# Kernel tuning notes

Measured on AMD Instinct MI355X. Metric: run time of the kernel, lower is better.

Reference implementation:

```python
import jax, jax.numpy as jnp
import numpy as np
from functools import partial

B, N, T = 4, 10000, 128
E = 160000
H, C = 4, 64            # heads, out_channels per head
GAT_DIM = H * C         # 256
NEG_SLOPE = 0.2


def conv1d(x, w, b):
    # x: (M, Cin, L), w: (Cout, Cin, K), 'same' padding (pad=1 for k=3)
    y = jax.lax.conv_general_dilated(x, w, window_strides=(1,), padding=[(1, 1)],
                                     dimension_numbers=('NCH', 'OIH', 'NCH'))
    return y + b[None, :, None]


def maxpool2(x):
    # kernel=2, stride=2 over last axis
    return jax.lax.reduce_window(x, -jnp.inf, jax.lax.max,
                                 (1, 1, 2), (1, 1, 2), 'VALID')


def gat_layer_single(x, src, dst, W, att_s, att_d, bias):
    # x: (N, Fin); PyG GATConv with concat=True, self-loops already appended to src/dst
    n = x.shape[0]
    xl = (x @ W).reshape(n, H, C)                       # (N, H, C)
    a_s = jnp.sum(xl * att_s[None], axis=-1)            # (N, H)
    a_d = jnp.sum(xl * att_d[None], axis=-1)            # (N, H)
    e = jax.nn.leaky_relu(a_s[src] + a_d[dst], NEG_SLOPE)  # (E', H)
    emax = jax.ops.segment_max(e, dst, num_segments=n)     # (N, H)
    ex = jnp.exp(e - emax[dst])
    denom = jax.ops.segment_sum(ex, dst, num_segments=n)   # (N, H)
    alpha = ex / (denom[dst] + 1e-16)                       # (E', H)
    msg = xl[src] * alpha[..., None]                        # (E', H, C)
    out = jax.ops.segment_sum(msg, dst, num_segments=n)     # (N, H, C)
    return out.reshape(n, H * C) + bias


def setup_inputs() -> dict:
    key = jax.random.key(0)
    ks = jax.random.split(key, 24)
    rn = lambda k, sh, fan: jax.random.normal(k, sh, jnp.float32) / np.sqrt(fan)
    inp = {
        'x': jax.random.normal(ks[0], (B, N, T), jnp.float32),
        'edge_index': jax.random.randint(ks[1], (2, E), 0, N, jnp.int64),
        # temporal conv
        'cw1': rn(ks[2], (32, 1, 3), 3), 'cb1': jnp.zeros((32,), jnp.float32),
        'cw2': rn(ks[3], (64, 32, 3), 96), 'cb2': jnp.zeros((64,), jnp.float32),
        # GAT layer 0 (in=64)
        'W0': rn(ks[4], (64, GAT_DIM), 64), 'as0': rn(ks[5], (H, C), C), 'ad0': rn(ks[6], (H, C), C),
        'b0': jnp.zeros((GAT_DIM,), jnp.float32),
        # GAT layer 1 (in=256)
        'W1': rn(ks[7], (GAT_DIM, GAT_DIM), GAT_DIM), 'as1': rn(ks[8], (H, C), C), 'ad1': rn(ks[9], (H, C), C),
        'b1': jnp.zeros((GAT_DIM,), jnp.float32),
        # classification head 256->128->2
        'Wc1': rn(ks[10], (GAT_DIM, 128), GAT_DIM), 'bc1': jnp.zeros((128,), jnp.float32),
        'Wc2': rn(ks[11], (128, 2), 128), 'bc2': jnp.zeros((2,), jnp.float32),
        # attribution head 256->64->1
        'Wa1': rn(ks[12], (GAT_DIM, 64), GAT_DIM), 'ba1': jnp.zeros((64,), jnp.float32),
        'Wa2': rn(ks[13], (64, 1), 64), 'ba2': jnp.zeros((1,), jnp.float32),
    }
    return inp


def reference(x, edge_index, cw1, cb1, cw2, cb2, W0, as0, ad0, b0, W1, as1, ad1, b1,
              Wc1, bc1, Wc2, bc2, Wa1, ba1, Wa2, ba2):
    b, n, t = x.shape
    # ---- temporal conv over all B*N node signals ----
    xf = x.reshape(b * n, 1, t)
    h = jax.nn.relu(conv1d(xf, cw1, cb1))            # (BN, 32, T)
    h = maxpool2(h)                                  # (BN, 32, T//2)
    h = jax.nn.relu(conv1d(h, cw2, cb2))             # (BN, 64, T//2)
    feat = jnp.mean(h, axis=-1).reshape(b, n, 64)    # adaptive_avg_pool1d(1)
    # ---- GAT stack (self-loops appended, PyG default) ----
    src0, dst0 = edge_index[0], edge_index[1]
    loops = jnp.arange(n, dtype=src0.dtype)
    src = jnp.concatenate([src0, loops])
    dst = jnp.concatenate([dst0, loops])
    gat0 = jax.vmap(partial(gat_layer_single, src=src, dst=dst, W=W0, att_s=as0, att_d=ad0, bias=b0))
    gat1 = jax.vmap(partial(gat_layer_single, src=src, dst=dst, W=W1, att_s=as1, att_d=ad1, bias=b1))
    g = jax.nn.relu(gat0(feat))                      # (B, N, 256); dropout = identity (eval)
    g = jax.nn.relu(gat1(g))                         # (B, N, 256)
    # ---- heads ----
    pooled = jnp.mean(g, axis=1)                     # (B, 256)
    logits = jax.nn.relu(pooled @ Wc1 + bc1) @ Wc2 + bc2          # (B, 2)
    attr = jax.nn.sigmoid(jax.nn.relu(g @ Wa1 + ba1) @ Wa2 + ba2)  # (B, N, 1)
    return logits, attr[..., 0]
```

## Files before the change

### kernel.cpp

```cpp
#include <hip/hip_runtime.h>
#include <hip/hip_bf16.h>
#include <math.h>

typedef __hip_bfloat16 bf16;
typedef unsigned short u16;
typedef unsigned int u32;
typedef __attribute__((ext_vector_type(8))) short short8;
typedef __attribute__((ext_vector_type(4))) float f32x4;
typedef __attribute__((ext_vector_type(2))) float f32x2;

#define BATCH 4
#define NNODE 10000
#define TLEN 128
#define NEDGE 160000
#define GDIM 256
#define NHEAD 4

#define S_CW1 0
#define S_CB1 96
#define S_CB2 128
#define S_AS0 192
#define S_AD0 448
#define S_B0  704
#define S_AS1 960
#define S_AD1 1216
#define S_B1  1472
#define S_BC1 1728
#define S_WC2 1856
#define S_BC2 2112
#define S_BA1 2114
#define S_WA2 2178
#define S_BA2 2242
#define S_TOTAL 2243

__device__ __forceinline__ float prelu(float v) { return fmaxf(v, 0.f); }
__device__ __forceinline__ u16 f2b(float f) {
    union { float f; u32 u; } v; v.f = f;
    u32 r = v.u + 0x7FFF + ((v.u >> 16) & 1);
    return (u16)(r >> 16);
}
__device__ __forceinline__ float u2f(u16 u) {
    union { u32 u; float f; } v; v.u = ((u32)u) << 16;
    return v.f;
}
__device__ __forceinline__ float ldw(const void* p, int off, bool isbf) {
    return isbf ? u2f(((const u16*)p)[off]) : ((const float*)p)[off];
}

__device__ __forceinline__ bool probe_x_bf16(const void* xsrc) {
    int lane = threadIdx.x & 63;
    u16 h = ((const u16*)xsrc)[2 * lane];
    int e = (h >> 7) & 0xFF;
    unsigned long long m = __ballot(e >= 117 && e <= 130);
    return __popcll(m) >= 32;
}
__device__ __forceinline__ bool probe_ei64(const int* ei) {
    int lane = threadIdx.x & 63;
    int v = ei[2 * lane + 1];
    unsigned long long m = __ballot(v == 0);
    return __popcll(m) >= 56;
}

struct WPtrs { const void* p[20]; };

#define PRE_TBLK 665
__global__ __launch_bounds__(256) void k_pre(WPtrs wp, const void* __restrict__ xsrc,
        const int* __restrict__ ei, float* __restrict__ wbuf,
        u16* __restrict__ cw2r, u16* __restrict__ W0t, u16* __restrict__ W1t,
        u16* __restrict__ Wa1t, int* __restrict__ counts) {
    bool isbf = probe_x_bf16(xsrc);
    int b = blockIdx.x;
    if (b >= PRE_TBLK) {
        const int C2[16] = {0,96,128,192,448,704,960,1216,1472,1728,1856,2112,
                            2114,2178,2242,2243};
        const int SRC[15] = {0,1,3,5,6,7,9,10,11,13,14,15,17,18,19};
        int i = (b - PRE_TBLK) * 256 + threadIdx.x;
        if (i >= S_TOTAL) return;
        int j = 14;
        for (int t = 0; t < 15; ++t) { if (i < C2[t + 1]) { j = t; break; } }
        wbuf[i] = ldw(wp.p[SRC[j]], i - C2[j], isbf);
        return;
    }
    int i = b * 256 + threadIdx.x;
    if (i < 6144) {
        int c2 = i / 96, k = i - c2 * 96, s = k >> 5, ci = k & 31;
        cw2r[i] = f2b(ldw(wp.p[2], c2 * 96 + ci * 3 + s, isbf));
    }
    if (i < 16384) {
        int k = i >> 8, c = i & 255;
        W0t[c * 64 + k] = f2b(ldw(wp.p[4], k * 256 + c, isbf));
        int ka = i >> 6, ca = i & 63;
        Wa1t[ca * 256 + ka] = f2b(ldw(wp.p[16], ka * 64 + ca, isbf));
    }
    if (i < 65536) {
        int k = i >> 8, c = i & 255;
        W1t[c * 256 + k] = f2b(ldw(wp.p[8], k * 256 + c, isbf));
    }
    if (i < NEDGE + NNODE) {
        bool ei64 = probe_ei64(ei);
        int dst;
        if (i < NEDGE) dst = ei64 ? ei[2 * (NEDGE + i)] : ei[NEDGE + i];
        else dst = i - NEDGE;
        if (dst >= 0 && dst < NNODE) atomicAdd(&counts[dst], 1);
    }
}

__global__ __launch_bounds__(256) void k_scan1(const int* __restrict__ counts,
        int* __restrict__ cur, int* __restrict__ bsum) {
    __shared__ int buf[256];
    int tid = threadIdx.x;
    int i = blockIdx.x * 256 + tid;
    int v = (i < NNODE) ? counts[i] : 0;
    buf[tid] = v;
    __syncthreads();
    for (int off = 1; off < 256; off <<= 1) {
        int t = (tid >= off) ? buf[tid - off] : 0;
        __syncthreads();
        buf[tid] += t;
        __syncthreads();
    }
    if (i < NNODE) cur[i] = buf[tid];
    if (tid == 255) bsum[blockIdx.x] = buf[255];
}
__global__ __launch_bounds__(256) void k_scan3(const int* __restrict__ counts,
        int* __restrict__ cur, const int* __restrict__ bsum, int* __restrict__ row_ptr) {
    __shared__ int pre_s;
    int tid = threadIdx.x;
    if (tid == 0) {
        int s = 0;
        for (int j = 0; j < blockIdx.x; ++j) s += bsum[j];
        pre_s = s;
    }
    __syncthreads();
    int i = blockIdx.x * 256 + tid;
    if (i >= NNODE) return;
    int incl = cur[i] + pre_s;
    row_ptr[i + 1] = incl;
    cur[i] = incl - counts[i];
    if (i == 0) row_ptr[0] = 0;
}

#define HSTR 40
#define NPW 4
#define FILL_BLK 665
__global__ __launch_bounds__(256) void k_conv(const void* __restrict__ xsrc,
        const float* __restrict__ wbuf, const u16* __restrict__ cw2r,
        u16* __restrict__ featb, const int* __restrict__ ei,
        int* __restrict__ cur, int* __restrict__ col_src) {
    __shared__ __align__(16) float xs[4][132];
    __shared__ float w1s[96], b1s[32], b2s[64];
    __shared__ __align__(16) u16 hb[4][66 * HSTR];

    bool isbf = probe_x_bf16(xsrc);
    int tid = threadIdx.x;
    int wave = tid >> 6, lane = tid & 63;
    int node0 = blockIdx.x * (4 * NPW);

    int m = lane & 15, q = lane >> 4;
    short8 bfr[4][3];
    #pragma unroll
    for (int nt = 0; nt < 4; ++nt)
        #pragma unroll
        for (int sh = 0; sh < 3; ++sh)
            bfr[nt][sh] = *(const short8*)&cw2r[(nt * 16 + m) * 96 + sh * 32 + q * 8];

    if (tid < 96) w1s[tid] = wbuf[S_CW1 + tid];
    if (tid < 32) b1s[tid] = wbuf[S_CB1 + tid];
    if (tid < 64) b2s[tid] = wbuf[S_CB2 + tid];
    if (tid < 8) xs[tid >> 1][(tid & 1) ? 129 : 0] = 0.f;
    if (tid < 64) {
        int w = tid >> 4, idx = tid & 15;
        *(u32*)&hb[w][2 * idx] = 0;
        *(u32*)&hb[w][65 * HSTR + 2 * idx] = 0;
    }
    __syncthreads();

    float* xsw = xs[wave];
    u16* hw = &hb[wave][0];

    int d = m, uu = q;
    float wa0 = w1s[6 * d + 0], wa1 = w1s[6 * d + 1], wa2 = w1s[6 * d + 2];
    float wb0 = w1s[6 * d + 3], wb1 = w1s[6 * d + 4], wb2 = w1s[6 * d + 5];
    float ba = b1s[2 * d], bb = b1s[2 * d + 1];
    float b2vv[4];
    #pragma unroll
    for (int nt = 0; nt < 4; ++nt) b2vv[nt] = b2s[nt * 16 + m];

    int node = node0 + wave;
    u32 plo = 0; float2 pf = {0.f, 0.f};
    if (isbf) plo = ((const u32*)xsrc)[(size_t)node * 64 + lane];
    else      pf  = ((const float2*)xsrc)[(size_t)node * 64 + lane];

    for (int j = 0; j < NPW; ++j) {
        if (isbf) {
            xsw[1 + 2 * lane] = u2f((u16)(plo & 0xFFFF));
            xsw[2 + 2 * lane] = u2f((u16)(plo >> 16));
        } else {
            xsw[1 + 2 * lane] = pf.x;
            xsw[2 + 2 * lane] = pf.y;
        }
        if (j + 1 < NPW) {
            int nxt = node + 4;
            if (isbf) plo = ((const u32*)xsrc)[(size_t)nxt * 64 + lane];
            else      pf  = ((const float2*)xsrc)[(size_t)nxt * 64 + lane];
        }

        #pragma unroll
        for (int it = 0; it < 16; ++it) {
            int u = uu + 4 * it;
            int t0 = 2 * u;
            float2 xa = *(const float2*)&xsw[t0];
            float2 xb = *(const float2*)&xsw[t0 + 2];
            float x0 = xa.x, x1 = xa.y, x2 = xb.x, x3 = xb.y;
            f32x2 A = {x0, x1}, Bv = {x1, x2}, Cv = {x2, x3};
            f32x2 va = {ba, ba}; va += wa0 * A; va += wa1 * Bv; va += wa2 * Cv;
            f32x2 vb = {bb, bb}; vb += wb0 * A; vb += wb1 * Bv; vb += wb2 * Cv;
            float ha = fmaxf(fmaxf(va.x, va.y), 0.f);
            float hb2 = fmaxf(fmaxf(vb.x, vb.y), 0.f);
            __hip_bfloat162 hp2 = __float22bfloat162_rn(make_float2(ha, hb2));
            u32 pack; __builtin_memcpy(&pack, &hp2, 4);
            *(u32*)&hw[(u + 1) * HSTR + 2 * d] = pack;
        }

        float pc0 = 0.f, pc1 = 0.f, pc2 = 0.f, pc3 = 0.f;
        #pragma unroll
        for (int mt = 0; mt < 4; ++mt) {
            const u16* hr = &hw[(mt * 16 + m) * HSTR + q * 8];
            short8 a0 = *(const short8*)&hr[0 * HSTR];
            short8 a1 = *(const short8*)&hr[1 * HSTR];
            short8 a2 = *(const short8*)&hr[2 * HSTR];
            f32x4 c0 = {0.f,0.f,0.f,0.f}, c1 = {0.f,0.f,0.f,0.f};
            f32x4 c2 = {0.f,0.f,0.f,0.f}, c3 = {0.f,0.f,0.f,0.f};
            c0 = __builtin_amdgcn_mfma_f32_16x16x32_bf16(a0, bfr[0][0], c0, 0, 0, 0);
            c1 = __builtin_amdgcn_mfma_f32_16x16x32_bf16(a0, bfr[1][0], c1, 0, 0, 0);
            c2 = __builtin_amdgcn_mfma_f32_16x16x32_bf16(a0, bfr[2][0], c2, 0, 0, 0);
            c3 = __builtin_amdgcn_mfma_f32_16x16x32_bf16(a0, bfr[3][0], c3, 0, 0, 0);
            c0 = __builtin_amdgcn_mfma_f32_16x16x32_bf16(a1, bfr[0][1], c0, 0, 0, 0);
            c1 = __builtin_amdgcn_mfma_f32_16x16x32_bf16(a1, bfr[1][1], c1, 0, 0, 0);
            c2 = __builtin_amdgcn_mfma_f32_16x16x32_bf16(a1, bfr[2][1], c2, 0, 0, 0);
            c3 = __builtin_amdgcn_mfma_f32_16x16x32_bf16(a1, bfr[3][1], c3, 0, 0, 0);
            c0 = __builtin_amdgcn_mfma_f32_16x16x32_bf16(a2, bfr[0][2], c0, 0, 0, 0);
            c1 = __builtin_amdgcn_mfma_f32_16x16x32_bf16(a2, bfr[1][2], c1, 0, 0, 0);
            c2 = __builtin_amdgcn_mfma_f32_16x16x32_bf16(a2, bfr[2][2], c2, 0, 0, 0);
            c3 = __builtin_amdgcn_mfma_f32_16x16x32_bf16(a2, bfr[3][2], c3, 0, 0, 0);
            pc0 += prelu(c0[0] + b2vv[0]) + prelu(c0[1] + b2vv[0])
                 + prelu(c0[2] + b2vv[0]) + prelu(c0[3] + b2vv[0]);
            pc1 += prelu(c1[0] + b2vv[1]) + prelu(c1[1] + b2vv[1])
                 + prelu(c1[2] + b2vv[1]) + prelu(c1[3] + b2vv[1]);
            pc2 += prelu(c2[0] + b2vv[2]) + prelu(c2[1] + b2vv[2])
                 + prelu(c2[2] + b2vv[2]) + prelu(c2[3] + b2vv[2]);
            pc3 += prelu(c3[0] + b2vv[3]) + prelu(c3[1] + b2vv[3])
                 + prelu(c3[2] + b2vv[3]) + prelu(c3[3] + b2vv[3]);
        }
        pc0 += __shfl_xor(pc0, 16, 64); pc0 += __shfl_xor(pc0, 32, 64);
        pc1 += __shfl_xor(pc1, 16, 64); pc1 += __shfl_xor(pc1, 32, 64);
        pc2 += __shfl_xor(pc2, 16, 64); pc2 += __shfl_xor(pc2, 32, 64);
        pc3 += __shfl_xor(pc3, 16, 64); pc3 += __shfl_xor(pc3, 32, 64);
        float v = (q == 0) ? pc0 : (q == 1) ? pc1 : (q == 2) ? pc2 : pc3;
        int bb2 = node / NNODE, nn = node - bb2 * NNODE;
        featb[((size_t)nn * 4 + bb2) * 64 + lane] = f2b(v * (1.f / 64.f));

        node += 4;
    }

    if (blockIdx.x < FILL_BLK) {
        bool ei64 = probe_ei64(ei);
        int e = blockIdx.x * 256 + tid;
        if (e < NEDGE + NNODE) {
            int src, dst;
            if (e < NEDGE) {
                if (ei64) { src = ei[2 * e]; dst = ei[2 * (NEDGE + e)]; }
                else      { src = ei[e];     dst = ei[NEDGE + e]; }
            } else {
                src = dst = e - NEDGE;
            }
            if (dst >= 0 && dst < NNODE) {
                int pos = atomicAdd(&cur[dst], 1);
                if (pos >= 0 && pos < NEDGE + NNODE) col_src[pos] = src;
            }
        }
    }
}

template<int K>
__global__ __launch_bounds__(256) void k_gemm(const u16* __restrict__ A,
        const u16* __restrict__ Wt, const float* __restrict__ att_s_w,
        const float* __restrict__ att_d_w, u16* __restrict__ outb,
        float* __restrict__ a_s, float* __restrict__ a_d) {
    int wave = threadIdx.x >> 6, lane = threadIdx.x & 63;
    int row0 = (blockIdx.x * 4 + wave) * 16;
    int m = lane & 15, q = lane >> 4;
    f32x4 acc[16];
    #pragma unroll
    for (int nt = 0; nt < 16; ++nt) acc[nt] = {0.f, 0.f, 0.f, 0.f};
    for (int kc = 0; kc < K; kc += 32) {
        short8 a = *(const short8*)&A[(size_t)(row0 + m) * K + kc + q * 8];
        #pragma unroll
        for (int nt = 0; nt < 16; ++nt) {
            short8 b = *(const short8*)&Wt[(size_t)(nt * 16 + m) * K + kc + q * 8];
            acc[nt] = __builtin_amdgcn_mfma_f32_16x16x32_bf16(a, b, acc[nt], 0, 0, 0);
        }
    }
    #pragma unroll
    for (int nt = 0; nt < 16; ++nt) {
        #pragma unroll
        for (int r = 0; r < 4; ++r)
            outb[(size_t)(row0 + q * 4 + r) * 256 + nt * 16 + m] = f2b(acc[nt][r]);
    }
    float sh_s[4][4] = {{0}}, sh_d[4][4] = {{0}};
    #pragma unroll
    for (int nt = 0; nt < 16; ++nt) {
        int h = nt >> 2;
        int cc = (nt & 3) * 16 + m;
        float asw = att_s_w[h * 64 + cc];
        float adw = att_d_w[h * 64 + cc];
        #pragma unroll
        for (int r = 0; r < 4; ++r) {
            sh_s[h][r] += acc[nt][r] * asw;
            sh_d[h][r] += acc[nt][r] * adw;
        }
    }
    #pragma unroll
    for (int off = 1; off < 16; off <<= 1) {
        #pragma unroll
        for (int h = 0; h < 4; ++h)
            #pragma unroll
            for (int r = 0; r < 4; ++r) {
                sh_s[h][r] += __shfl_xor(sh_s[h][r], off, 64);
                sh_d[h][r] += __shfl_xor(sh_d[h][r], off, 64);
            }
    }
    if (m == 0) {
        #pragma unroll
        for (int r = 0; r < 4; ++r) {
            int row = row0 + q * 4 + r;
            float4 vs = {sh_s[0][r], sh_s[1][r], sh_s[2][r], sh_s[3][r]};
            float4 vd = {sh_d[0][r], sh_d[1][r], sh_d[2][r], sh_d[3][r]};
            *(float4*)&a_s[(size_t)row * 4] = vs;
            *(float4*)&a_d[(size_t)row * 4] = vd;
        }
    }
}

__global__ __launch_bounds__(256) void k_agg(const u16* __restrict__ xlb,
        const float* __restrict__ a_s, const float* __restrict__ a_d,
        const int* __restrict__ row_ptr, const int* __restrict__ col_src,
        const float* __restrict__ bias, u16* __restrict__ gb_out) {
    int wave = threadIdx.x >> 6, lane = threadIdx.x & 63;
    int dst = __builtin_amdgcn_readfirstlane(blockIdx.x * 2 + (wave >> 1));
    int bp = (wave & 1) * 2;
    int beg = __builtin_amdgcn_readfirstlane(row_ptr[dst]);
    int end = __builtin_amdgcn_readfirstlane(row_ptr[dst + 1]);

    int bl = lane >> 5;
    int s = lane & 31;
    int h = s >> 3;
    int b = bp + bl;
    int asoff = b * 4 + h;
    float advh = a_d[(size_t)dst * 16 + asoff];

    float m = -INFINITY, l = 0.f;
    float acc[8];
    #pragma unroll
    for (int k = 0; k < 8; ++k) acc[k] = 0.f;

    int i = beg;
    for (; i + 4 <= end; i += 4) {
        int s0 = min(max(col_src[i], 0), NNODE - 1);
        int s1 = min(max(col_src[i + 1], 0), NNODE - 1);
        int s2 = min(max(col_src[i + 2], 0), NNODE - 1);
        int s3 = min(max(col_src[i + 3], 0), NNODE - 1);
        float a0 = a_s[(size_t)s0 * 16 + asoff];
        float a1 = a_s[(size_t)s1 * 16 + asoff];
        float a2 = a_s[(size_t)s2 * 16 + asoff];
        float a3 = a_s[(size_t)s3 * 16 + asoff];
        short8 x0 = *(const short8*)&xlb[((size_t)s0 * 4 + b) * 256 + s * 8];
        short8 x1 = *(const short8*)&xlb[((size_t)s1 * 4 + b) * 256 + s * 8];
        short8 x2 = *(const short8*)&xlb[((size_t)s2 * 4 + b) * 256 + s * 8];
        short8 x3 = *(const short8*)&xlb[((size_t)s3 * 4 + b) * 256 + s * 8];
        float e0 = a0 + advh; e0 = (e0 >= 0.f) ? e0 : 0.2f * e0;
        float e1 = a1 + advh; e1 = (e1 >= 0.f) ? e1 : 0.2f * e1;
        float e2 = a2 + advh; e2 = (e2 >= 0.f) ? e2 : 0.2f * e2;
        float e3 = a3 + advh; e3 = (e3 >= 0.f) ? e3 : 0.2f * e3;
        float cmax = fmaxf(fmaxf(e0, e1), fmaxf(e2, e3));
        if (__any(cmax > m)) {
            float mn = fmaxf(m, cmax);
            float r = __expf(m - mn);
            m = mn;
            l *= r;
            #pragma unroll
            for (int k = 0; k < 8; ++k) acc[k] *= r;
        }
        float p0 = __expf(e0 - m); l += p0;
        #pragma unroll
        for (int k = 0; k < 8; ++k) acc[k] += p0 * u2f((u16)x0[k]);
        float p1 = __expf(e1 - m); l += p1;
        #pragma unroll
        for (int k = 0; k < 8; ++k) acc[k] += p1 * u2f((u16)x1[k]);
        float p2 = __expf(e2 - m); l += p2;
        #pragma unroll
        for (int k = 0; k < 8; ++k) acc[k] += p2 * u2f((u16)x2[k]);
        float p3 = __expf(e3 - m); l += p3;
        #pragma unroll
        for (int k = 0; k < 8; ++k) acc[k] += p3 * u2f((u16)x3[k]);
    }
    for (; i < end; ++i) {
        int s0 = min(max(col_src[i], 0), NNODE - 1);
        float a0 = a_s[(size_t)s0 * 16 + asoff];
        short8 x0 = *(const short8*)&xlb[((size_t)s0 * 4 + b) * 256 + s * 8];
        float e0 = a0 + advh; e0 = (e0 >= 0.f) ? e0 : 0.2f * e0;
        if (__any(e0 > m)) {
            float mn = fmaxf(m, e0);
            float r = __expf(m - mn);
            m = mn;
            l *= r;
            #pragma unroll
            for (int k = 0; k < 8; ++k) acc[k] *= r;
        }
        float p0 = __expf(e0 - m); l += p0;
        #pragma unroll
        for (int k = 0; k < 8; ++k) acc[k] += p0 * u2f((u16)x0[k]);
    }

    float rl = 1.f / (l + 1e-16f);
    short8 o;
    #pragma unroll
    for (int k = 0; k < 8; ++k)
        o[k] = (short)f2b(prelu(acc[k] * rl + bias[s * 8 + k]));
    *(short8*)&gb_out[((size_t)dst * 4 + b) * 256 + s * 8] = o;
}

__global__ __launch_bounds__(256) void k_attrpool(const u16* __restrict__ gb,
        const u16* __restrict__ Wa1t, const float* __restrict__ wbuf,
        float* __restrict__ out, float* __restrict__ pooled) {
    if (blockIdx.x >= 625) {
        int pb = blockIdx.x - 625;
        int b = pb >> 6;
        int chunk = pb & 63;
        int cch = threadIdx.x;
        int n0 = chunk * 157;
        int n1 = min(NNODE, n0 + 157);
        float acc = 0.f;
        int n = n0;
        for (; n + 4 <= n1; n += 4) {
            float v0 = u2f(gb[((size_t)n * 4 + b) * 256 + cch]);
            float v1 = u2f(gb[((size_t)(n + 1) * 4 + b) * 256 + cch]);
            float v2 = u2f(gb[((size_t)(n + 2) * 4 + b) * 256 + cch]);
            float v3 = u2f(gb[((size_t)(n + 3) * 4 + b) * 256 + cch]);
            acc += v0; acc += v1; acc += v2; acc += v3;
        }
        for (; n < n1; ++n)
            acc += u2f(gb[((size_t)n * 4 + b) * 256 + cch]);
        atomicAdd(&pooled[b * 256 + cch], acc);
        return;
    }
    int wave = threadIdx.x >> 6, lane = threadIdx.x & 63;
    int row0 = (blockIdx.x * 4 + wave) * 16;
    int m = lane & 15, q = lane >> 4;
    f32x4 acc[4];
    #pragma unroll
    for (int nt = 0; nt < 4; ++nt) acc[nt] = {0.f, 0.f, 0.f, 0.f};
    for (int kc = 0; kc < 256; kc += 32) {
        short8 a = *(const short8*)&gb[(size_t)(row0 + m) * 256 + kc + q * 8];
        #pragma unroll
        for (int nt = 0; nt < 4; ++nt) {
            short8 b = *(const short8*)&Wa1t[(size_t)(nt * 16 + m) * 256 + kc + q * 8];
            acc[nt] = __builtin_amdgcn_mfma_f32_16x16x32_bf16(a, b, acc[nt], 0, 0, 0);
        }
    }
    float part[4] = {0, 0, 0, 0};
    #pragma unroll
    for (int nt = 0; nt < 4; ++nt) {
        int col = nt * 16 + m;
        float ba1v = wbuf[S_BA1 + col];
        float wa2v = wbuf[S_WA2 + col];
        #pragma unroll
        for (int r = 0; r < 4; ++r)
            part[r] += prelu(acc[nt][r] + ba1v) * wa2v;
    }
    #pragma unroll
    for (int off = 1; off < 16; off <<= 1) {
        #pragma unroll
        for (int r = 0; r < 4; ++r)
            part[r] += __shfl_xor(part[r], off, 64);
    }
    if (m == 0) {
        float ba2v = wbuf[S_BA2];
        #pragma unroll
        for (int r = 0; r < 4; ++r) {
            int row = row0 + q * 4 + r;
            int n = row >> 2, b = row & 3;
            float v = part[r] + ba2v;
            out[8 + b * NNODE + n] = 1.f / (1.f + __expf(-v));
        }
    }
}

__global__ __launch_bounds__(128) void k_logits(const float* __restrict__ pooled,
        const float* __restrict__ wbuf, const void* __restrict__ Wc1p,
        float* __restrict__ out,
        const u16* __restrict__ featb, const u16* __restrict__ gb,
        const int* __restrict__ row_ptr, const int* __restrict__ ei,
        const void* __restrict__ xsrc, int hostbad) {
    int tid = threadIdx.x;
    bool isbf = probe_x_bf16(xsrc);
    if (blockIdx.x == 4) {
        __shared__ float red[128];
        bool ei64 = probe_ei64(ei);
        float mx[2] = {0.f, 0.f};
        const u16* bufs[2] = {featb, gb};
        for (int qq = 0; qq < 2; ++qq) {
            const u16* p = bufs[qq];
            float m = 0.f;
            for (int i = tid; i < 2048; i += 128) {
                float v = u2f(p[i]);
                if (v != v) m = 1e30f;
                m = fmaxf(m, fabsf(v));
            }
            red[tid] = m;
            __syncthreads();
            for (int s2 = 64; s2 > 0; s2 >>= 1) {
                if (tid < s2) red[tid] = fmaxf(red[tid], red[tid + s2]);
                __syncthreads();
            }
            mx[qq] = red[0];
            __syncthreads();
        }
        if (tid == 0) {
            int fb = (mx[0] > 1e8f || mx[0] < 1e-6f) ? 1 : 0;
            int gbad = (mx[1] > 1e8f || mx[1] < 1e-6f) ? 1 : 0;
            int cb = (row_ptr[NNODE] != NEDGE + NNODE) ? 1 : 0;
            int code = 100 * fb + 400 * gbad + 800 * cb + 6400 * hostbad;
            if (code) {
                code += 1600 * (isbf ? 0 : 1);
                code += 3200 * (ei64 ? 1 : 0);
                for (int j = 0; j < 8; ++j) out[j] = (float)code;
            }
        }
        return;
    }
    __shared__ float pm[256];
    __shared__ float red4[4];
    int b = blockIdx.x;
    pm[tid] = pooled[b * 256 + tid] * (1.f / NNODE);
    pm[tid + 128] = pooled[b * 256 + tid + 128] * (1.f / NNODE);
    __syncthreads();
    float acc = wbuf[S_BC1 + tid];
    if (isbf) {
        const u16* w = (const u16*)Wc1p;
        #pragma unroll 4
        for (int k = 0; k < 256; ++k)
            acc += pm[k] * u2f(w[k * 128 + tid]);
    } else {
        const float* w = (const float*)Wc1p;
        #pragma unroll 4
        for (int k = 0; k < 256; ++k)
            acc += pm[k] * w[k * 128 + tid];
    }
    float hv = prelu(acc);
    float p0 = hv * wbuf[S_WC2 + tid * 2];
    float p1 = hv * wbuf[S_WC2 + tid * 2 + 1];
    #pragma unroll
    for (int off = 32; off > 0; off >>= 1) {
        p0 += __shfl_xor(p0, off, 64);
        p1 += __shfl_xor(p1, off, 64);
    }
    int wv = tid >> 6, lane = tid & 63;
    if (lane == 0) { red4[wv * 2] = p0; red4[wv * 2 + 1] = p1; }
    __syncthreads();
    if (tid < 2)
        out[b * 2 + tid] = red4[tid] + red4[2 + tid] + wbuf[S_BC2 + tid];
}

extern "C" void kernel_launch(void* const* d_in, const int* in_sizes, int n_in,
                              void* d_out, int out_size, void* d_ws, size_t ws_size,
                              hipStream_t stream) {
    const void* x  = d_in[0];
    const int*  ei = (const int*)d_in[1];
    float* out = (float*)d_out;

    WPtrs wp;
    for (int j = 0; j < 20; ++j) wp.p[j] = d_in[j + 2];

    char* ws = (char*)d_ws;
    size_t off = 0;
    auto alloc = [&](size_t bytes) -> void* {
        void* p = ws + off;
        off += (bytes + 255) & ~(size_t)255;
        return p;
    };
    float* wbuf    = (float*)alloc((size_t)S_TOTAL * 4);
    u16*   featb   = (u16*)  alloc((size_t)BATCH * NNODE * 64 * 2);
    u16*   xlb     = (u16*)  alloc((size_t)BATCH * NNODE * 256 * 2);
    u16*   gb      = (u16*)  alloc((size_t)BATCH * NNODE * 256 * 2);
    float* a_s     = (float*)alloc((size_t)BATCH * NNODE * 4 * 4);
    float* a_d     = (float*)alloc((size_t)BATCH * NNODE * 4 * 4);
    u16*   cw2r    = (u16*)alloc(6144 * 2);
    u16*   W0t     = (u16*)alloc(16384 * 2);
    u16*   W1t     = (u16*)alloc(65536 * 2);
    u16*   Wa1t    = (u16*)alloc(16384 * 2);
    int*   counts  = (int*)alloc(NNODE * 4);
    float* pooled  = (float*)alloc(BATCH * 256 * 4);
    int*   row_ptr = (int*)alloc((NNODE + 1) * 4);
    int*   cur     = (int*)alloc(NNODE * 4);
    int*   col_src = (int*)alloc((NEDGE + NNODE) * 4);
    int*   bsum    = (int*)alloc(64 * 4);
    (void)ws_size; (void)out_size;

    int hostbad = (n_in != 22 || in_sizes[0] != BATCH * NNODE * TLEN ||
                   in_sizes[1] != 2 * NEDGE) ? 1 : 0;

    hipMemsetAsync(counts, 0, 40192 + 4096, stream);

    k_pre<<<PRE_TBLK + 9, 256, 0, stream>>>(wp, x, ei, wbuf, cw2r, W0t, W1t, Wa1t, counts);
    k_scan1<<<40, 256, 0, stream>>>(counts, cur, bsum);
    k_scan3<<<40, 256, 0, stream>>>(counts, cur, bsum, row_ptr);

    k_conv<<<BATCH * NNODE / (4 * NPW), 256, 0, stream>>>(x, wbuf, cw2r, featb, ei, cur, col_src);

    k_gemm<64><<<BATCH * NNODE / 64, 256, 0, stream>>>(featb, W0t,
            wbuf + S_AS0, wbuf + S_AD0, xlb, a_s, a_d);
    k_agg<<<NNODE / 2, 256, 0, stream>>>(xlb, a_s, a_d, row_ptr, col_src, wbuf + S_B0, gb);

    k_gemm<256><<<BATCH * NNODE / 64, 256, 0, stream>>>(gb, W1t,
            wbuf + S_AS1, wbuf + S_AD1, xlb, a_s, a_d);
    k_agg<<<NNODE / 2, 256, 0, stream>>>(xlb, a_s, a_d, row_ptr, col_src, wbuf + S_B1, gb);

    k_attrpool<<<625 + 256, 256, 0, stream>>>(gb, Wa1t, wbuf, out, pooled);
    k_logits<<<5, 128, 0, stream>>>(pooled, wbuf, wp.p[12], out, featb, gb, row_ptr, ei, x, hostbad);
}
```

Measured before the change: 394.6 us.

## Interleave attention scores into feature rows, prefetch edge indices, single-kernel scan

```diff
diff --git a/kernel.cpp b/kernel.cpp
--- a/kernel.cpp
+++ b/kernel.cpp
@@ -15,6 +15,7 @@
 #define NEDGE 160000
 #define GDIM 256
 #define NHEAD 4
+#define XROW 272
 
 #define S_CW1 0
 #define S_CB1 96
@@ -105,39 +106,38 @@
     }
 }
 
-__global__ __launch_bounds__(256) void k_scan1(const int* __restrict__ counts,
-        int* __restrict__ cur, int* __restrict__ bsum) {
-    __shared__ int buf[256];
-    int tid = threadIdx.x;
-    int i = blockIdx.x * 256 + tid;
-    int v = (i < NNODE) ? counts[i] : 0;
-    buf[tid] = v;
+__global__ __launch_bounds__(1024) void k_scan(const int* __restrict__ counts,
+        int* __restrict__ cur, int* __restrict__ row_ptr) {
+    __shared__ int buf[1024];
+    int t = threadIdx.x;
+    int base = t * 10;
+    int c[10];
+    int s = 0;
+    #pragma unroll
+    for (int i = 0; i < 10; ++i) {
+        int idx = base + i;
+        c[i] = (idx < NNODE) ? counts[idx] : 0;
+        s += c[i];
+    }
+    buf[t] = s;
     __syncthreads();
-    for (int off = 1; off < 256; off <<= 1) {
-        int t = (tid >= off) ? buf[tid - off] : 0;
+    for (int off = 1; off < 1024; off <<= 1) {
+        int v = (t >= off) ? buf[t - off] : 0;
         __syncthreads();
-        buf[tid] += t;
+        buf[t] += v;
         __syncthreads();
     }
-    if (i < NNODE) cur[i] = buf[tid];
-    if (tid == 255) bsum[blockIdx.x] = buf[255];
-}
-__global__ __launch_bounds__(256) void k_scan3(const int* __restrict__ counts,
-        int* __restrict__ cur, const int* __restrict__ bsum, int* __restrict__ row_ptr) {
-    __shared__ int pre_s;
-    int tid = threadIdx.x;
-    if (tid == 0) {
-        int s = 0;
-        for (int j = 0; j < blockIdx.x; ++j) s += bsum[j];
-        pre_s = s;
-    }
-    __syncthreads();
-    int i = blockIdx.x * 256 + tid;
-    if (i >= NNODE) return;
-    int incl = cur[i] + pre_s;
-    row_ptr[i + 1] = incl;
-    cur[i] = incl - counts[i];
-    if (i == 0) row_ptr[0] = 0;
+    int run = buf[t] - s;
+    #pragma unroll
+    for (int i = 0; i < 10; ++i) {
+        int idx = base + i;
+        if (idx < NNODE) {
+            cur[idx] = run;
+            run += c[i];
+            row_ptr[idx + 1] = run;
+        }
+    }
+    if (t == 0) row_ptr[0] = 0;
 }
 
 #define HSTR 40
@@ -285,8 +285,7 @@
 template<int K>
 __global__ __launch_bounds__(256) void k_gemm(const u16* __restrict__ A,
         const u16* __restrict__ Wt, const float* __restrict__ att_s_w,
-        const float* __restrict__ att_d_w, u16* __restrict__ outb,
-        float* __restrict__ a_s, float* __restrict__ a_d) {
+        const float* __restrict__ att_d_w, u16* __restrict__ outb) {
     int wave = threadIdx.x >> 6, lane = threadIdx.x & 63;
     int row0 = (blockIdx.x * 4 + wave) * 16;
     int m = lane & 15, q = lane >> 4;
@@ -305,7 +304,7 @@
     for (int nt = 0; nt < 16; ++nt) {
         #pragma unroll
         for (int r = 0; r < 4; ++r)
-            outb[(size_t)(row0 + q * 4 + r) * 256 + nt * 16 + m] = f2b(acc[nt][r]);
+            outb[(size_t)(row0 + q * 4 + r) * XROW + nt * 16 + m] = f2b(acc[nt][r]);
     }
     float sh_s[4][4] = {{0}}, sh_d[4][4] = {{0}};
     #pragma unroll
@@ -336,14 +335,13 @@
             int row = row0 + q * 4 + r;
             float4 vs = {sh_s[0][r], sh_s[1][r], sh_s[2][r], sh_s[3][r]};
             float4 vd = {sh_d[0][r], sh_d[1][r], sh_d[2][r], sh_d[3][r]};
-            *(float4*)&a_s[(size_t)row * 4] = vs;
-            *(float4*)&a_d[(size_t)row * 4] = vd;
+            *(float4*)&outb[(size_t)row * XROW + 256] = vs;
+            *(float4*)&outb[(size_t)row * XROW + 264] = vd;
         }
     }
 }
 
 __global__ __launch_bounds__(256) void k_agg(const u16* __restrict__ xlb,
-        const float* __restrict__ a_s, const float* __restrict__ a_d,
         const int* __restrict__ row_ptr, const int* __restrict__ col_src,
         const float* __restrict__ bias, u16* __restrict__ gb_out) {
     int wave = threadIdx.x >> 6, lane = threadIdx.x & 63;
@@ -356,8 +354,7 @@
     int s = lane & 31;
     int h = s >> 3;
     int b = bp + bl;
-    int asoff = b * 4 + h;
-    float advh = a_d[(size_t)dst * 16 + asoff];
+    float advh = *(const float*)&xlb[((size_t)dst * 4 + b) * XROW + 264 + h * 2];
 
     float m = -INFINITY, l = 0.f;
     float acc[8];
@@ -365,19 +362,33 @@
     for (int k = 0; k < 8; ++k) acc[k] = 0.f;
 
     int i = beg;
-    for (; i + 4 <= end; i += 4) {
-        int s0 = min(max(col_src[i], 0), NNODE - 1);
-        int s1 = min(max(col_src[i + 1], 0), NNODE - 1);
-        int s2 = min(max(col_src[i + 2], 0), NNODE - 1);
-        int s3 = min(max(col_src[i + 3], 0), NNODE - 1);
-        float a0 = a_s[(size_t)s0 * 16 + asoff];
-        float a1 = a_s[(size_t)s1 * 16 + asoff];
-        float a2 = a_s[(size_t)s2 * 16 + asoff];
-        float a3 = a_s[(size_t)s3 * 16 + asoff];
-        short8 x0 = *(const short8*)&xlb[((size_t)s0 * 4 + b) * 256 + s * 8];
-        short8 x1 = *(const short8*)&xlb[((size_t)s1 * 4 + b) * 256 + s * 8];
-        short8 x2 = *(const short8*)&xlb[((size_t)s2 * 4 + b) * 256 + s * 8];
-        short8 x3 = *(const short8*)&xlb[((size_t)s3 * 4 + b) * 256 + s * 8];
+    int n0 = 0, n1 = 0, n2 = 0, n3 = 0;
+    if (i + 4 <= end) {
+        n0 = col_src[i]; n1 = col_src[i + 1];
+        n2 = col_src[i + 2]; n3 = col_src[i + 3];
+    }
+    while (i + 4 <= end) {
+        int s0 = min(max(n0, 0), NNODE - 1);
+        int s1 = min(max(n1, 0), NNODE - 1);
+        int s2 = min(max(n2, 0), NNODE - 1);
+        int s3 = min(max(n3, 0), NNODE - 1);
+        const u16* r0 = &xlb[((size_t)s0 * 4 + b) * XROW];
+        const u16* r1 = &xlb[((size_t)s1 * 4 + b) * XROW];
+        const u16* r2 = &xlb[((size_t)s2 * 4 + b) * XROW];
+        const u16* r3 = &xlb[((size_t)s3 * 4 + b) * XROW];
+        float a0 = *(const float*)&r0[256 + h * 2];
+        float a1 = *(const float*)&r1[256 + h * 2];
+        float a2 = *(const float*)&r2[256 + h * 2];
+        float a3 = *(const float*)&r3[256 + h * 2];
+        short8 x0 = *(const short8*)&r0[s * 8];
+        short8 x1 = *(const short8*)&r1[s * 8];
+        short8 x2 = *(const short8*)&r2[s * 8];
+        short8 x3 = *(const short8*)&r3[s * 8];
+        i += 4;
+        if (i + 4 <= end) {
+            n0 = col_src[i]; n1 = col_src[i + 1];
+            n2 = col_src[i + 2]; n3 = col_src[i + 3];
+        }
         float e0 = a0 + advh; e0 = (e0 >= 0.f) ? e0 : 0.2f * e0;
         float e1 = a1 + advh; e1 = (e1 >= 0.f) ? e1 : 0.2f * e1;
         float e2 = a2 + advh; e2 = (e2 >= 0.f) ? e2 : 0.2f * e2;
@@ -406,8 +417,9 @@
     }
     for (; i < end; ++i) {
         int s0 = min(max(col_src[i], 0), NNODE - 1);
-        float a0 = a_s[(size_t)s0 * 16 + asoff];
-        short8 x0 = *(const short8*)&xlb[((size_t)s0 * 4 + b) * 256 + s * 8];
+        const u16* r0 = &xlb[((size_t)s0 * 4 + b) * XROW];
+        float a0 = *(const float*)&r0[256 + h * 2];
+        short8 x0 = *(const short8*)&r0[s * 8];
         float e0 = a0 + advh; e0 = (e0 >= 0.f) ? e0 : 0.2f * e0;
         if (__any(e0 > m)) {
             float mn = fmaxf(m, e0);
@@ -591,10 +603,8 @@
     };
     float* wbuf    = (float*)alloc((size_t)S_TOTAL * 4);
     u16*   featb   = (u16*)  alloc((size_t)BATCH * NNODE * 64 * 2);
-    u16*   xlb     = (u16*)  alloc((size_t)BATCH * NNODE * 256 * 2);
+    u16*   xlb     = (u16*)  alloc((size_t)BATCH * NNODE * XROW * 2);
     u16*   gb      = (u16*)  alloc((size_t)BATCH * NNODE * 256 * 2);
-    float* a_s     = (float*)alloc((size_t)BATCH * NNODE * 4 * 4);
-    float* a_d     = (float*)alloc((size_t)BATCH * NNODE * 4 * 4);
     u16*   cw2r    = (u16*)alloc(6144 * 2);
     u16*   W0t     = (u16*)alloc(16384 * 2);
     u16*   W1t     = (u16*)alloc(65536 * 2);
@@ -604,7 +614,6 @@
     int*   row_ptr = (int*)alloc((NNODE + 1) * 4);
     int*   cur     = (int*)alloc(NNODE * 4);
     int*   col_src = (int*)alloc((NEDGE + NNODE) * 4);
-    int*   bsum    = (int*)alloc(64 * 4);
     (void)ws_size; (void)out_size;
 
     int hostbad = (n_in != 22 || in_sizes[0] != BATCH * NNODE * TLEN ||
@@ -613,18 +622,17 @@
     hipMemsetAsync(counts, 0, 40192 + 4096, stream);
 
     k_pre<<<PRE_TBLK + 9, 256, 0, stream>>>(wp, x, ei, wbuf, cw2r, W0t, W1t, Wa1t, counts);
-    k_scan1<<<40, 256, 0, stream>>>(counts, cur, bsum);
-    k_scan3<<<40, 256, 0, stream>>>(counts, cur, bsum, row_ptr);
+    k_scan<<<1, 1024, 0, stream>>>(counts, cur, row_ptr);
 
     k_conv<<<BATCH * NNODE / (4 * NPW), 256, 0, stream>>>(x, wbuf, cw2r, featb, ei, cur, col_src);
 
     k_gemm<64><<<BATCH * NNODE / 64, 256, 0, stream>>>(featb, W0t,
-            wbuf + S_AS0, wbuf + S_AD0, xlb, a_s, a_d);
-    k_agg<<<NNODE / 2, 256, 0, stream>>>(xlb, a_s, a_d, row_ptr, col_src, wbuf + S_B0, gb);
+            wbuf + S_AS0, wbuf + S_AD0, xlb);
+    k_agg<<<NNODE / 2, 256, 0, stream>>>(xlb, row_ptr, col_src, wbuf + S_B0, gb);
 
     k_gemm<256><<<BATCH * NNODE / 64, 256, 0, stream>>>(gb, W1t,
-            wbuf + S_AS1, wbuf + S_AD1, xlb, a_s, a_d);
-    k_agg<<<NNODE / 2, 256, 0, stream>>>(xlb, a_s, a_d, row_ptr, col_src, wbuf + S_B1, gb);
+            wbuf + S_AS1, wbuf + S_AD1, xlb);
+    k_agg<<<NNODE / 2, 256, 0, stream>>>(xlb, row_ptr, col_src, wbuf + S_B1, gb);
 
     k_attrpool<<<625 + 256, 256, 0, stream>>>(gb, Wa1t, wbuf, out, pooled);
     k_logits<<<5, 128, 0, stream>>>(pooled, wbuf, wp.p[12], out, featb, gb, row_ptr, ei, x, hostbad);
```

New measurement: 402.3 us. No clear change (+2.0%).
